# Kernel tuning notes

Hardware: AMD Instinct MI355X
Metric: run time of the kernel (lower is better)

## Reference

```python
import jax, jax.numpy as jnp
import numpy as np

ALPHA = 0.2          # LeakyReLU negative slope
NEG_INF = -9e15      # mask fill value used by the torch module


def setup_inputs() -> dict:
    key = jax.random.key(0)
    k1, k2, k3, k4 = jax.random.split(key, 4)
    N, F_IN, F_OUT = 1024, 64, 64
    h = jax.random.normal(k1, (N, F_IN), dtype=jnp.float32)
    # adj > 0 marks edges; random 0/1 dense adjacency (diag not required: all-masked rows
    # softmax to uniform, matching torch semantics with the finite -9e15 fill)
    adj = jax.random.randint(k2, (N, N), 0, 2, dtype=jnp.int32)
    # xavier_uniform(gain=1.414) equivalents
    lim_W = 1.414 * np.sqrt(6.0 / (F_IN + F_OUT))
    W = jax.random.uniform(k3, (F_IN, F_OUT), minval=-lim_W, maxval=lim_W, dtype=jnp.float32)
    lim_a = 1.414 * np.sqrt(6.0 / (2 * F_OUT + 1))
    a = jax.random.uniform(k4, (2 * F_OUT, 1), minval=-lim_a, maxval=lim_a, dtype=jnp.float32)
    return {"h": h, "adj": adj, "W": W, "a": a}


def reference(h, adj, W, a):
    F_OUT = W.shape[1]
    Wh = h @ W                                   # (N, F_out)
    # a^T [Wh_i || Wh_j] decomposes: e_ij = (Wh @ a1)_i + (Wh @ a2)_j  -- same math,
    # without materializing the (N, N, 2F) concat tensor.
    a1, a2 = a[:F_OUT, 0], a[F_OUT:, 0]
    e = (Wh @ a1)[:, None] + (Wh @ a2)[None, :]  # (N, N)
    e = jax.nn.leaky_relu(e, negative_slope=ALPHA)
    scores = jnp.where(adj > 0, e, jnp.float32(NEG_INF))
    attention = jax.nn.softmax(scores, axis=1)   # dropout is identity at eval
    h_prime = attention @ Wh                     # (N, F_out)
    return jax.nn.elu(h_prime)                   # concat=True branch
```

## Files before the change

### kernel.cpp

```cpp
#include <hip/hip_runtime.h>

#define ALPHA 0.2f

constexpr int N = 1024;
constexpr int F = 64;
constexpr int TI = 4;
constexpr int NT = 1024;
constexpr int NW = NT / 64;

__global__ __launch_bounds__(256) void k1e(const float* __restrict__ h,
                                           const float* __restrict__ W,
                                           const float* __restrict__ a,
                                           float* __restrict__ e1,
                                           float* __restrict__ e2) {
    const int t = threadIdx.x;
    __shared__ float w1s[F], w2s[F];

    {
        const int f = t >> 2;
        const int c0 = (t & 3) * 16;
        float s1 = 0.f, s2 = 0.f;
        #pragma unroll
        for (int q = 0; q < 4; ++q) {
            const float4 wv  = *(const float4*)&W[f * F + c0 + q * 4];
            const float4 a1v = *(const float4*)&a[c0 + q * 4];
            const float4 a2v = *(const float4*)&a[F + c0 + q * 4];
            s1 += wv.x*a1v.x + wv.y*a1v.y + wv.z*a1v.z + wv.w*a1v.w;
            s2 += wv.x*a2v.x + wv.y*a2v.y + wv.z*a2v.z + wv.w*a2v.w;
        }
        s1 += __shfl_down(s1, 2); s1 += __shfl_down(s1, 1);
        s2 += __shfl_down(s2, 2); s2 += __shfl_down(s2, 1);
        if ((t & 3) == 0) { w1s[f] = s1; w2s[f] = s2; }
    }
    __syncthreads();

    const int wave = t >> 6;
    const int lane = t & 63;
    const int i = blockIdx.x * 4 + wave;
    const float hv = h[(size_t)i * F + lane];
    float v1 = hv * w1s[lane];
    float v2 = hv * w2s[lane];
    #pragma unroll
    for (int off = 32; off > 0; off >>= 1) {
        v1 += __shfl_down(v1, off);
        v2 += __shfl_down(v2, off);
    }
    if (lane == 0) {
        e1[i] = v1;
        e2[i] = v2;
    }
}

__global__ __launch_bounds__(NT) void k2e(const int* __restrict__ adj,
                                          const float* __restrict__ h,
                                          const float* __restrict__ W,
                                          const float* __restrict__ e1,
                                          const float* __restrict__ e2,
                                          float* __restrict__ out) {
    const int i0 = blockIdx.x * TI;
    const int t = threadIdx.x;
    const int wave = t >> 6;
    const int lane = t & 63;

    __shared__ float e2s[N];
    __shared__ float e1s[TI];
    __shared__ float p[TI][N];
    __shared__ float accs[NW][TI][F];
    __shared__ float redsum[NW];
    __shared__ float us[TI][F];

    const int r = t >> 8;
    const int j4 = (t & 255) * 4;
    const int4 av = *(const int4*)&adj[(size_t)(i0 + r) * N + j4];

    e2s[t] = e2[t];
    if (t < TI) e1s[t] = e1[i0 + t];
    __syncthreads();

    {
        const float e1r = e1s[r];
        const float4 ev = *(const float4*)&e2s[j4];
        float4 pe;
        float s;
        s = e1r + ev.x; s = (s > 0.f) ? s : ALPHA * s; pe.x = (av.x > 0) ? __expf(s) : 0.f;
        s = e1r + ev.y; s = (s > 0.f) ? s : ALPHA * s; pe.y = (av.y > 0) ? __expf(s) : 0.f;
        s = e1r + ev.z; s = (s > 0.f) ? s : ALPHA * s; pe.z = (av.z > 0) ? __expf(s) : 0.f;
        s = e1r + ev.w; s = (s > 0.f) ? s : ALPHA * s; pe.w = (av.w > 0) ? __expf(s) : 0.f;
        *(float4*)&p[r][j4] = pe;
        float ls = (pe.x + pe.y) + (pe.z + pe.w);
        #pragma unroll
        for (int off = 32; off > 0; off >>= 1) ls += __shfl_down(ls, off);
        if (lane == 0) redsum[wave] = ls;
    }
    __syncthreads();

    {
        float a0 = 0.f, a1 = 0.f, a2 = 0.f, a3 = 0.f;
        const int j0 = wave * 64;
        #pragma unroll 4
        for (int j = j0; j < j0 + 64; j += 4) {
            const float4 p0 = *(const float4*)&p[0][j];
            const float4 p1 = *(const float4*)&p[1][j];
            const float4 p2 = *(const float4*)&p[2][j];
            const float4 p3 = *(const float4*)&p[3][j];
            #pragma unroll
            for (int u = 0; u < 4; ++u) {
                const float hv = h[(size_t)(j + u) * F + lane];
                a0 += (&p0.x)[u] * hv;
                a1 += (&p1.x)[u] * hv;
                a2 += (&p2.x)[u] * hv;
                a3 += (&p3.x)[u] * hv;
            }
        }
        accs[wave][0][lane] = a0;
        accs[wave][1][lane] = a1;
        accs[wave][2][lane] = a2;
        accs[wave][3][lane] = a3;
    }
    __syncthreads();

    if (t < TI * F) {
        const int rr = t >> 6;
        const int f = t & 63;
        float su = 0.f;
        #pragma unroll
        for (int w = 0; w < NW; ++w) su += accs[w][rr][f];
        const float dn = redsum[4*rr] + redsum[4*rr+1] + redsum[4*rr+2] + redsum[4*rr+3];
        us[rr][f] = su / dn;
    }
    __syncthreads();

    if (t < TI * F) {
        const int rr = t >> 6;
        const int g = t & 63;
        float acc = 0.f;
        #pragma unroll
        for (int f = 0; f < F; ++f)
            acc += us[rr][f] * W[f * F + g];
        out[(size_t)(i0 + rr) * F + g] = (acc > 0.f) ? acc : expm1f(acc);
    }
}

extern "C" void kernel_launch(void* const* d_in, const int* in_sizes, int n_in,
                              void* d_out, int out_size, void* d_ws, size_t ws_size,
                              hipStream_t stream) {
    const float* h   = (const float*)d_in[0];
    const int*   adj = (const int*)d_in[1];
    const float* W   = (const float*)d_in[2];
    const float* a   = (const float*)d_in[3];
    float* out       = (float*)d_out;

    float* ws = (float*)d_ws;
    float* e1 = ws;
    float* e2 = ws + N;

    k1e<<<256, 256, 0, stream>>>(h, W, a, e1, e2);
    k2e<<<N / TI, NT, 0, stream>>>(adj, h, W, e1, e2, out);
}
```

Measured before the change: 69.55 us.

## Fuse score projection into attention kernel and make per-wave stages barrier-free

Merges the two launches into one kernel. Each block recomputes W·a1 and W·a2, and each wave computes e2 for its own 64 columns directly from h, so the workspace round trip and the second launch go away. Each wave's softmax numerators stay in a per-wave shared slice, and the intermediate stages use waitcnt instead of block barriers. The cost is redundant e2 and W·a work in every one of the 256 blocks, plus reliance on wave-local LDS ordering.

```diff
diff --git a/kernel.cpp b/kernel.cpp
--- a/kernel.cpp
+++ b/kernel.cpp
@@ -8,152 +8,149 @@
 constexpr int NT = 1024;
 constexpr int NW = NT / 64;
 
-__global__ __launch_bounds__(256) void k1e(const float* __restrict__ h,
-                                           const float* __restrict__ W,
-                                           const float* __restrict__ a,
-                                           float* __restrict__ e1,
-                                           float* __restrict__ e2) {
-    const int t = threadIdx.x;
-    __shared__ float w1s[F], w2s[F];
+__global__ __launch_bounds__(NT) void gat_fused(
+    const float* __restrict__ h,
+    const int* __restrict__ adj,
+    const float* __restrict__ W,
+    const float* __restrict__ a,
+    float* __restrict__ out) {
 
-    {
-        const int f = t >> 2;
-        const int c0 = (t & 3) * 16;
-        float s1 = 0.f, s2 = 0.f;
-        #pragma unroll
-        for (int q = 0; q < 4; ++q) {
-            const float4 wv  = *(const float4*)&W[f * F + c0 + q * 4];
-            const float4 a1v = *(const float4*)&a[c0 + q * 4];
-            const float4 a2v = *(const float4*)&a[F + c0 + q * 4];
-            s1 += wv.x*a1v.x + wv.y*a1v.y + wv.z*a1v.z + wv.w*a1v.w;
-            s2 += wv.x*a2v.x + wv.y*a2v.y + wv.z*a2v.z + wv.w*a2v.w;
-        }
-        s1 += __shfl_down(s1, 2); s1 += __shfl_down(s1, 1);
-        s2 += __shfl_down(s2, 2); s2 += __shfl_down(s2, 1);
-        if ((t & 3) == 0) { w1s[f] = s1; w2s[f] = s2; }
+  const int t = threadIdx.x;
+  const int wave = t >> 6;
+  const int lane = t & 63;
+  const int i0 = blockIdx.x * TI;
+  const int j = t;
+
+  __shared__ float w1s[F], w2s[F];
+  __shared__ float e2s[NW][64];
+  __shared__ float pws[NW][TI][64];
+  __shared__ float accs[NW][TI][F];
+  __shared__ float us[TI][F];
+
+  int ad[TI];
+  float hvr[TI];
+  #pragma unroll
+  for (int r = 0; r < TI; ++r) {
+    ad[r]  = adj[(size_t)(i0 + r) * N + j];
+    hvr[r] = h[(size_t)(i0 + r) * F + lane];
+  }
+
+  if (t < 256) {
+    const int f = t >> 2;
+    const int c0 = (t & 3) * 16;
+    float s1 = 0.f, s2 = 0.f;
+    #pragma unroll
+    for (int q = 0; q < 4; ++q) {
+      const float4 wv  = *(const float4*)&W[f * F + c0 + q * 4];
+      const float4 a1v = *(const float4*)&a[c0 + q * 4];
+      const float4 a2v = *(const float4*)&a[F + c0 + q * 4];
+      s1 += wv.x*a1v.x + wv.y*a1v.y + wv.z*a1v.z + wv.w*a1v.w;
+      s2 += wv.x*a2v.x + wv.y*a2v.y + wv.z*a2v.z + wv.w*a2v.w;
     }
-    __syncthreads();
+    s1 += __shfl_down(s1, 2); s1 += __shfl_down(s1, 1);
+    s2 += __shfl_down(s2, 2); s2 += __shfl_down(s2, 1);
+    if ((t & 3) == 0) { w1s[f] = s1; w2s[f] = s2; }
+  }
+  __syncthreads();
 
-    const int wave = t >> 6;
-    const int lane = t & 63;
-    const int i = blockIdx.x * 4 + wave;
-    const float hv = h[(size_t)i * F + lane];
-    float v1 = hv * w1s[lane];
-    float v2 = hv * w2s[lane];
+  float e1r[TI];
+  #pragma unroll
+  for (int r = 0; r < TI; ++r) {
+    float v = hvr[r] * w1s[lane];
     #pragma unroll
-    for (int off = 32; off > 0; off >>= 1) {
-        v1 += __shfl_down(v1, off);
-        v2 += __shfl_down(v2, off);
+    for (int off = 32; off > 0; off >>= 1) v += __shfl_xor(v, off);
+    e1r[r] = v;
+  }
+
+  {
+    const int sub = lane >> 2;
+    const int qf  = (lane & 3) << 4;
+    #pragma unroll
+    for (int pass = 0; pass < 4; ++pass) {
+      const int row = (wave << 6) + (pass << 4) + sub;
+      const float* hr = &h[(size_t)row * F + qf];
+      float s = 0.f;
+      #pragma unroll
+      for (int q = 0; q < 4; ++q) {
+        const float4 hv = *(const float4*)&hr[q * 4];
+        const float4 wv = *(const float4*)&w2s[qf + q * 4];
+        s += hv.x*wv.x + hv.y*wv.y + hv.z*wv.z + hv.w*wv.w;
+      }
+      s += __shfl_down(s, 2);
+      s += __shfl_down(s, 1);
+      if ((lane & 3) == 0) e2s[wave][(pass << 4) + sub] = s;
     }
-    if (lane == 0) {
-        e1[i] = v1;
-        e2[i] = v2;
+  }
+  asm volatile("s_waitcnt lgkmcnt(0)" ::: "memory");
+  const float e2v = e2s[wave][lane];
+
+  #pragma unroll
+  for (int r = 0; r < TI; ++r) {
+    float s = e1r[r] + e2v;
+    s = (s > 0.f) ? s : ALPHA * s;
+    pws[wave][r][lane] = (ad[r] > 0) ? __expf(s) : 0.f;
+  }
+  asm volatile("s_waitcnt lgkmcnt(0)" ::: "memory");
+
+  {
+    float a0 = 0.f, a1 = 0.f, a2 = 0.f, a3 = 0.f;
+    const float* hb = h + (size_t)(wave << 6) * F + lane;
+    #pragma unroll 4
+    for (int jc = 0; jc < 64; jc += 4) {
+      const float4 q0 = *(const float4*)&pws[wave][0][jc];
+      const float4 q1 = *(const float4*)&pws[wave][1][jc];
+      const float4 q2 = *(const float4*)&pws[wave][2][jc];
+      const float4 q3 = *(const float4*)&pws[wave][3][jc];
+      #pragma unroll
+      for (int u = 0; u < 4; ++u) {
+        const float hv = hb[(size_t)(jc + u) * F];
+        a0 += (&q0.x)[u] * hv;
+        a1 += (&q1.x)[u] * hv;
+        a2 += (&q2.x)[u] * hv;
+        a3 += (&q3.x)[u] * hv;
+      }
     }
-}
+    accs[wave][0][lane] = a0;
+    accs[wave][1][lane] = a1;
+    accs[wave][2][lane] = a2;
+    accs[wave][3][lane] = a3;
+  }
+  __syncthreads();
 
-__global__ __launch_bounds__(NT) void k2e(const int* __restrict__ adj,
-                                          const float* __restrict__ h,
-                                          const float* __restrict__ W,
-                                          const float* __restrict__ e1,
-                                          const float* __restrict__ e2,
-                                          float* __restrict__ out) {
-    const int i0 = blockIdx.x * TI;
-    const int t = threadIdx.x;
-    const int wave = t >> 6;
-    const int lane = t & 63;
+  if (t < TI * F) {
+    const int rr = t >> 6;
+    const int f = t & 63;
+    float su = 0.f, ps = 0.f;
+    #pragma unroll
+    for (int w = 0; w < NW; ++w) {
+      su += accs[w][rr][f];
+      ps += pws[w][rr][f];
+    }
+    #pragma unroll
+    for (int off = 32; off > 0; off >>= 1) ps += __shfl_xor(ps, off);
+    us[rr][f] = su / ps;
+  }
+  __syncthreads();
 
-    __shared__ float e2s[N];
-    __shared__ float e1s[TI];
-    __shared__ float p[TI][N];
-    __shared__ float accs[NW][TI][F];
-    __shared__ float redsum[NW];
-    __shared__ float us[TI][F];
-
-    const int r = t >> 8;
-    const int j4 = (t & 255) * 4;
-    const int4 av = *(const int4*)&adj[(size_t)(i0 + r) * N + j4];
-
-    e2s[t] = e2[t];
-    if (t < TI) e1s[t] = e1[i0 + t];
-    __syncthreads();
-
-    {
-        const float e1r = e1s[r];
-        const float4 ev = *(const float4*)&e2s[j4];
-        float4 pe;
-        float s;
-        s = e1r + ev.x; s = (s > 0.f) ? s : ALPHA * s; pe.x = (av.x > 0) ? __expf(s) : 0.f;
-        s = e1r + ev.y; s = (s > 0.f) ? s : ALPHA * s; pe.y = (av.y > 0) ? __expf(s) : 0.f;
-        s = e1r + ev.z; s = (s > 0.f) ? s : ALPHA * s; pe.z = (av.z > 0) ? __expf(s) : 0.f;
-        s = e1r + ev.w; s = (s > 0.f) ? s : ALPHA * s; pe.w = (av.w > 0) ? __expf(s) : 0.f;
-        *(float4*)&p[r][j4] = pe;
-        float ls = (pe.x + pe.y) + (pe.z + pe.w);
-        #pragma unroll
-        for (int off = 32; off > 0; off >>= 1) ls += __shfl_down(ls, off);
-        if (lane == 0) redsum[wave] = ls;
-    }
-    __syncthreads();
-
-    {
-        float a0 = 0.f, a1 = 0.f, a2 = 0.f, a3 = 0.f;
-        const int j0 = wave * 64;
-        #pragma unroll 4
-        for (int j = j0; j < j0 + 64; j += 4) {
-            const float4 p0 = *(const float4*)&p[0][j];
-            const float4 p1 = *(const float4*)&p[1][j];
-            const float4 p2 = *(const float4*)&p[2][j];
-            const float4 p3 = *(const float4*)&p[3][j];
-            #pragma unroll
-            for (int u = 0; u < 4; ++u) {
-                const float hv = h[(size_t)(j + u) * F + lane];
-                a0 += (&p0.x)[u] * hv;
-                a1 += (&p1.x)[u] * hv;
-                a2 += (&p2.x)[u] * hv;
-                a3 += (&p3.x)[u] * hv;
-            }
-        }
-        accs[wave][0][lane] = a0;
-        accs[wave][1][lane] = a1;
-        accs[wave][2][lane] = a2;
-        accs[wave][3][lane] = a3;
-    }
-    __syncthreads();
-
-    if (t < TI * F) {
-        const int rr = t >> 6;
-        const int f = t & 63;
-        float su = 0.f;
-        #pragma unroll
-        for (int w = 0; w < NW; ++w) su += accs[w][rr][f];
-        const float dn = redsum[4*rr] + redsum[4*rr+1] + redsum[4*rr+2] + redsum[4*rr+3];
-        us[rr][f] = su / dn;
-    }
-    __syncthreads();
-
-    if (t < TI * F) {
-        const int rr = t >> 6;
-        const int g = t & 63;
-        float acc = 0.f;
-        #pragma unroll
-        for (int f = 0; f < F; ++f)
-            acc += us[rr][f] * W[f * F + g];
-        out[(size_t)(i0 + rr) * F + g] = (acc > 0.f) ? acc : expm1f(acc);
-    }
+  if (t < TI * F) {
+    const int rr = t >> 6;
+    const int g = t & 63;
+    float acc = 0.f;
+    #pragma unroll
+    for (int f = 0; f < F; ++f)
+      acc += us[rr][f] * W[f * F + g];
+    out[(size_t)(i0 + rr) * F + g] = (acc > 0.f) ? acc : expm1f(acc);
+  }
 }
 
 extern "C" void kernel_launch(void* const* d_in, const int* in_sizes, int n_in,
                               void* d_out, int out_size, void* d_ws, size_t ws_size,
                               hipStream_t stream) {
-    const float* h   = (const float*)d_in[0];
-    const int*   adj = (const int*)d_in[1];
-    const float* W   = (const float*)d_in[2];
-    const float* a   = (const float*)d_in[3];
-    float* out       = (float*)d_out;
+  const float* h   = (const float*)d_in[0];
+  const int*   adj = (const int*)d_in[1];
+  const float* W   = (const float*)d_in[2];
+  const float* a   = (const float*)d_in[3];
+  float* out       = (float*)d_out;
 
-    float* ws = (float*)d_ws;
-    float* e1 = ws;
-    float* e2 = ws + N;
-
-    k1e<<<256, 256, 0, stream>>>(h, W, a, e1, e2);
-    k2e<<<N / TI, NT, 0, stream>>>(adj, h, W, e1, e2, out);
+  gat_fused<<<N / TI, NT, 0, stream>>>(h, adj, W, a, out);
 }
```

Measured after the change: 71.02 us. 2.1% more time.

## Split attention aggregation into 2D row/column tiles with a separate finalize kernel

Applied to the files above, without the earlier changes.

The aggregation kernel now tiles 16 rows by 256 columns per block, so each h row loaded is reused across 16 attention rows instead of 4. This cuts redundant global reads of h. The per-wave softmax probabilities stay in wave-private LDS, and a waitcnt replaces a block barrier. Partial sums and denominators go to workspace, and a third kernel reduces them, normalizes, applies W and ELU. The cost is an extra launch and a workspace round trip.

```diff
diff --git a/kernel.cpp b/kernel.cpp
--- a/kernel.cpp
+++ b/kernel.cpp
@@ -4,9 +4,6 @@
 
 constexpr int N = 1024;
 constexpr int F = 64;
-constexpr int TI = 4;
-constexpr int NT = 1024;
-constexpr int NW = NT / 64;
 
 __global__ __launch_bounds__(256) void k1e(const float* __restrict__ h,
                                            const float* __restrict__ W,
@@ -51,94 +48,121 @@
     }
 }
 
-__global__ __launch_bounds__(NT) void k2e(const int* __restrict__ adj,
-                                          const float* __restrict__ h,
-                                          const float* __restrict__ W,
-                                          const float* __restrict__ e1,
-                                          const float* __restrict__ e2,
-                                          float* __restrict__ out) {
-    const int i0 = blockIdx.x * TI;
+__global__ __launch_bounds__(1024) void k2p(const int* __restrict__ adj,
+                                            const float* __restrict__ h,
+                                            const float* __restrict__ e1,
+                                            const float* __restrict__ e2,
+                                            float* __restrict__ wsu,
+                                            float* __restrict__ wsd) {
     const int t = threadIdx.x;
     const int wave = t >> 6;
     const int lane = t & 63;
+    const int ig = blockIdx.x >> 2;
+    const int jg = blockIdx.x & 3;
+    const int i0 = ig * 16;
+    const int j0 = jg * 256;
 
-    __shared__ float e2s[N];
-    __shared__ float e1s[TI];
-    __shared__ float p[TI][N];
-    __shared__ float accs[NW][TI][F];
-    __shared__ float redsum[NW];
-    __shared__ float us[TI][F];
+    __shared__ float e1s[16];
+    __shared__ float e2s[256];
+    __shared__ float pws[16][16][16];
+    __shared__ float accs[16][16][64];
+    __shared__ float dens[16][16];
 
-    const int r = t >> 8;
-    const int j4 = (t & 255) * 4;
-    const int4 av = *(const int4*)&adj[(size_t)(i0 + r) * N + j4];
+    const int r  = lane & 15;
+    const int hi = lane >> 4;
 
-    e2s[t] = e2[t];
-    if (t < TI) e1s[t] = e1[i0 + t];
+    const int4 av = *(const int4*)&adj[(size_t)(i0 + r) * N + j0 + wave * 16 + hi * 4];
+
+    if (t < 256) e2s[t] = e2[j0 + t];
+    if (t < 16)  e1s[t] = e1[i0 + t];
     __syncthreads();
 
     {
         const float e1r = e1s[r];
-        const float4 ev = *(const float4*)&e2s[j4];
-        float4 pe;
-        float s;
-        s = e1r + ev.x; s = (s > 0.f) ? s : ALPHA * s; pe.x = (av.x > 0) ? __expf(s) : 0.f;
-        s = e1r + ev.y; s = (s > 0.f) ? s : ALPHA * s; pe.y = (av.y > 0) ? __expf(s) : 0.f;
-        s = e1r + ev.z; s = (s > 0.f) ? s : ALPHA * s; pe.z = (av.z > 0) ? __expf(s) : 0.f;
-        s = e1r + ev.w; s = (s > 0.f) ? s : ALPHA * s; pe.w = (av.w > 0) ? __expf(s) : 0.f;
-        *(float4*)&p[r][j4] = pe;
-        float ls = (pe.x + pe.y) + (pe.z + pe.w);
+        const int jb = wave * 16 + hi * 4;
+        float4 pv; float s;
+        s = e1r + e2s[jb + 0]; s = (s > 0.f) ? s : ALPHA * s; pv.x = (av.x > 0) ? __expf(s) : 0.f;
+        s = e1r + e2s[jb + 1]; s = (s > 0.f) ? s : ALPHA * s; pv.y = (av.y > 0) ? __expf(s) : 0.f;
+        s = e1r + e2s[jb + 2]; s = (s > 0.f) ? s : ALPHA * s; pv.z = (av.z > 0) ? __expf(s) : 0.f;
+        s = e1r + e2s[jb + 3]; s = (s > 0.f) ? s : ALPHA * s; pv.w = (av.w > 0) ? __expf(s) : 0.f;
+        *(float4*)&pws[wave][r][hi * 4] = pv;
+        float d = (pv.x + pv.y) + (pv.z + pv.w);
+        d += __shfl_down(d, 32);
+        d += __shfl_down(d, 16);
+        if (lane < 16) dens[wave][lane] = d;
+    }
+    asm volatile("s_waitcnt lgkmcnt(0)" ::: "memory");
+
+    {
+        float u[16];
         #pragma unroll
-        for (int off = 32; off > 0; off >>= 1) ls += __shfl_down(ls, off);
-        if (lane == 0) redsum[wave] = ls;
+        for (int rr = 0; rr < 16; ++rr) u[rr] = 0.f;
+        const float* hb = h + (size_t)(j0 + wave * 16) * F + lane;
+        #pragma unroll
+        for (int g4 = 0; g4 < 4; ++g4) {
+            float hv[4];
+            #pragma unroll
+            for (int q = 0; q < 4; ++q)
+                hv[q] = hb[(size_t)(g4 * 4 + q) * F];
+            #pragma unroll
+            for (int rg = 0; rg < 4; ++rg) {
+                const float4 p0 = *(const float4*)&pws[wave][rg * 4 + 0][g4 * 4];
+                const float4 p1 = *(const float4*)&pws[wave][rg * 4 + 1][g4 * 4];
+                const float4 p2 = *(const float4*)&pws[wave][rg * 4 + 2][g4 * 4];
+                const float4 p3 = *(const float4*)&pws[wave][rg * 4 + 3][g4 * 4];
+                #pragma unroll
+                for (int q = 0; q < 4; ++q) {
+                    u[rg * 4 + 0] += (&p0.x)[q] * hv[q];
+                    u[rg * 4 + 1] += (&p1.x)[q] * hv[q];
+                    u[rg * 4 + 2] += (&p2.x)[q] * hv[q];
+                    u[rg * 4 + 3] += (&p3.x)[q] * hv[q];
+                }
+            }
+        }
+        #pragma unroll
+        for (int rr = 0; rr < 16; ++rr) accs[wave][rr][lane] = u[rr];
     }
     __syncthreads();
 
     {
-        float a0 = 0.f, a1 = 0.f, a2 = 0.f, a3 = 0.f;
-        const int j0 = wave * 64;
-        #pragma unroll 4
-        for (int j = j0; j < j0 + 64; j += 4) {
-            const float4 p0 = *(const float4*)&p[0][j];
-            const float4 p1 = *(const float4*)&p[1][j];
-            const float4 p2 = *(const float4*)&p[2][j];
-            const float4 p3 = *(const float4*)&p[3][j];
+        const int r2 = t >> 6;
+        const int f  = t & 63;
+        float su = 0.f;
+        #pragma unroll
+        for (int w = 0; w < 16; ++w) su += accs[w][r2][f];
+        wsu[(size_t)((i0 + r2) * 4 + jg) * 64 + f] = su;
+        if (t < 16) {
+            float d = 0.f;
             #pragma unroll
-            for (int u = 0; u < 4; ++u) {
-                const float hv = h[(size_t)(j + u) * F + lane];
-                a0 += (&p0.x)[u] * hv;
-                a1 += (&p1.x)[u] * hv;
-                a2 += (&p2.x)[u] * hv;
-                a3 += (&p3.x)[u] * hv;
-            }
+            for (int w = 0; w < 16; ++w) d += dens[w][t];
+            wsd[(i0 + t) * 4 + jg] = d;
         }
-        accs[wave][0][lane] = a0;
-        accs[wave][1][lane] = a1;
-        accs[wave][2][lane] = a2;
-        accs[wave][3][lane] = a3;
     }
+}
+
+__global__ __launch_bounds__(256) void k3f(const float* __restrict__ wsu,
+                                           const float* __restrict__ wsd,
+                                           const float* __restrict__ W,
+                                           float* __restrict__ out) {
+    const int t = threadIdx.x;
+    const int rr = t >> 6;
+    const int g  = t & 63;
+    const int i  = blockIdx.x * 4 + rr;
+    __shared__ float us[4][F];
+
+    float su = 0.f;
+    #pragma unroll
+    for (int jg = 0; jg < 4; ++jg)
+        su += wsu[(size_t)(i * 4 + jg) * 64 + g];
+    const float d = wsd[i * 4 + 0] + wsd[i * 4 + 1] + wsd[i * 4 + 2] + wsd[i * 4 + 3];
+    us[rr][g] = su / d;
     __syncthreads();
 
-    if (t < TI * F) {
-        const int rr = t >> 6;
-        const int f = t & 63;
-        float su = 0.f;
-        #pragma unroll
-        for (int w = 0; w < NW; ++w) su += accs[w][rr][f];
-        const float dn = redsum[4*rr] + redsum[4*rr+1] + redsum[4*rr+2] + redsum[4*rr+3];
-        us[rr][f] = su / dn;
-    }
-    __syncthreads();
-
-    if (t < TI * F) {
-        const int rr = t >> 6;
-        const int g = t & 63;
-        float acc = 0.f;
-        #pragma unroll
-        for (int f = 0; f < F; ++f)
-            acc += us[rr][f] * W[f * F + g];
-        out[(size_t)(i0 + rr) * F + g] = (acc > 0.f) ? acc : expm1f(acc);
-    }
+    float acc = 0.f;
+    #pragma unroll
+    for (int f = 0; f < F; ++f)
+        acc += us[rr][f] * W[f * F + g];
+    out[(size_t)i * F + g] = (acc > 0.f) ? acc : expm1f(acc);
 }
 
 extern "C" void kernel_launch(void* const* d_in, const int* in_sizes, int n_in,
@@ -150,10 +174,13 @@
     const float* a   = (const float*)d_in[3];
     float* out       = (float*)d_out;
 
-    float* ws = (float*)d_ws;
-    float* e1 = ws;
-    float* e2 = ws + N;
+    float* ws  = (float*)d_ws;
+    float* e1  = ws;
+    float* e2  = ws + N;
+    float* wsu = ws + 2 * N;
+    float* wsd = ws + 2 * N + N * 4 * F;
 
     k1e<<<256, 256, 0, stream>>>(h, W, a, e1, e2);
-    k2e<<<N / TI, NT, 0, stream>>>(adj, h, W, e1, e2, out);
+    k2p<<<256, 1024, 0, stream>>>(adj, h, e1, e2, wsu, wsd);
+    k3f<<<256, 256, 0, stream>>>(wsu, wsd, W, out);
 }
```

After: 72.85 us. 1.05x slower.
